# Performance work log

Hardware: AMD Instinct MI355X
Metric: run time of the kernel (lower is better)

Reference implementation:

```python
import jax, jax.numpy as jnp
import numpy as np
import math

B = 256          # batch size
D = 128          # input_size (embed dim)
N = 500000       # output_size == num_samples (memory bank rows)
K = 2048         # num_negative_samples
T = 0.07         # temperature
MOM = 0.5        # momentum
EPS = 1e-07


def _l2norm(x):
    return x / jnp.linalg.norm(x, axis=-1, keepdims=True)


def setup_inputs() -> dict:
    key = jax.random.key(0)
    k1, k2, k3, k4, k5, k6 = jax.random.split(key, 6)
    stdv = 1.0 / math.sqrt(D / 3.0)
    memory_v1 = jax.random.uniform(k1, (N, D), dtype=jnp.float32) * (2 * stdv) - stdv
    memory_v2 = jax.random.uniform(k2, (N, D), dtype=jnp.float32) * (2 * stdv) - stdv
    # embeds come out of an L2-normalization module in the original pipeline
    student_embed = _l2norm(jax.random.normal(k3, (B, D), dtype=jnp.float32))
    teacher_embed = _l2norm(jax.random.normal(k4, (B, D), dtype=jnp.float32))
    pos_idx = jax.random.randint(k5, (B,), 0, N, dtype=jnp.int64)
    contrast_idx = jax.random.randint(k6, (B, K + 1), 0, N, dtype=jnp.int64)
    contrast_idx = contrast_idx.at[:, 0].set(pos_idx)  # column 0 holds the positive
    return {
        'student_embed': student_embed,
        'teacher_embed': teacher_embed,
        'memory_v1': memory_v1,
        'memory_v2': memory_v2,
        'pos_idx': pos_idx,
        'contrast_idx': contrast_idx,
    }


def _contrast_loss(x):
    # x: [B, K+1] normalized exp-similarities; column 0 is the positive
    m = x.shape[1] - 1
    pn = 1.0 / float(N)  # num_samples
    noise = m * pn + EPS
    p_pos = x[:, 0]
    log_d1 = jnp.log(p_pos / (p_pos + noise))
    p_neg = x[:, 1:]
    log_d0 = jnp.log((m * pn) / (p_neg + noise))
    return -(log_d1.sum() + log_d0.sum()) / x.shape[0]


def reference(student_embed, teacher_embed, memory_v1, memory_v2, pos_idx, contrast_idx):
    output_size = memory_v1.shape[0]
    # gather [B, K+1, D] rows from each bank (detached in original)
    w1 = jax.lax.stop_gradient(memory_v1[contrast_idx])
    w2 = jax.lax.stop_gradient(memory_v2[contrast_idx])
    # per-sample bmm + exp/div  (teacher scored against v1 bank, student against v2)
    out_v2 = jnp.exp(jnp.einsum('bkd,bd->bk', w1, teacher_embed) / T)
    out_v1 = jnp.exp(jnp.einsum('bkd,bd->bk', w2, student_embed) / T)
    # first-call normalization constants (treated as constants thereafter)
    z_v1 = jax.lax.stop_gradient(out_v1.mean() * output_size)
    z_v2 = jax.lax.stop_gradient(out_v2.mean() * output_size)
    out_v1 = out_v1 / z_v1
    out_v2 = out_v2 / z_v2
    # momentum-weighted renormalize-and-scatter memory update (no_grad)
    s = jax.lax.stop_gradient(student_embed)
    t = jax.lax.stop_gradient(teacher_embed)
    l_pos = memory_v1[pos_idx] * MOM + s * (1.0 - MOM)
    updated_v1 = l_pos / jnp.sqrt((l_pos ** 2).sum(1, keepdims=True))
    new_memory_v1 = memory_v1.at[pos_idx].set(updated_v1)
    ab_pos = memory_v2[pos_idx] * MOM + t * (1.0 - MOM)
    updated_v2 = ab_pos / jnp.sqrt((ab_pos ** 2).sum(1, keepdims=True))
    new_memory_v2 = memory_v2.at[pos_idx].set(updated_v2)
    loss = _contrast_loss(out_v1) + _contrast_loss(out_v2)
    return loss, new_memory_v1, new_memory_v2
```

## Files before the change

### kernel.cpp

```cpp
#include <hip/hip_runtime.h>
#include <math.h>

namespace {
constexpr int kB = 256;
constexpr int kD = 128;
constexpr int kN = 500000;
constexpr int kKC = 2049;
constexpr int kNPair = kB * kKC;
constexpr float kTInv = 1.0f / 0.07f;
constexpr float kMom = 0.5f;
constexpr int kRB = 256;
constexpr long long kM = (long long)kN * kD;
constexpr long long kTot = 2 * kM;
constexpr int kChunk = 2048;
constexpr int kNB1 = (kN + kChunk - 1) / kChunk;
constexpr int kRows = 32;
constexpr int kTPB = kN / kRows;
constexpr int kTiles = 2 * kTPB;
constexpr int kLdsStride = 132;
constexpr int kTilesPerBlock = 16;
constexpr int kGrid8 = (kTiles + kTilesPerBlock - 1) / kTilesPerBlock;
}


__global__ __launch_bounds__(256) void hist_kernel(const int* __restrict__ cidx, int* __restrict__ A)
{
    int i = blockIdx.x * 256 + threadIdx.x;
    if (i < kNPair) atomicAdd(&A[cidx[i]], 1);
}

__global__ __launch_bounds__(256) void scan1_kernel(const int* __restrict__ A, int* __restrict__ bsum)
{
    long long base = (long long)blockIdx.x * kChunk;
    int t = threadIdx.x;
    int s = 0;
    #pragma unroll
    for (int j = 0; j < 8; ++j) {
        long long i = base + t * 8 + j;
        if (i < kN) s += A[i];
    }
    __shared__ int lds[256];
    lds[t] = s; __syncthreads();
    for (int st = 128; st > 0; st >>= 1) {
        if (t < st) lds[t] += lds[t + st];
        __syncthreads();
    }
    if (t == 0) bsum[blockIdx.x] = lds[0];
}

__global__ __launch_bounds__(256) void scan2_kernel(
    const int* __restrict__ bsum, int* __restrict__ bpre, int* __restrict__ offs)
{
    int t = threadIdx.x;
    int v = (t < kNB1) ? bsum[t] : 0;
    __shared__ int lds[256];
    lds[t] = v; __syncthreads();
    for (int st = 1; st < 256; st <<= 1) {
        int add = (t >= st) ? lds[t - st] : 0;
        __syncthreads();
        lds[t] += add;
        __syncthreads();
    }
    if (t < kNB1) bpre[t] = lds[t] - v;
    if (t == kNB1 - 1) offs[kN] = lds[t];
}

__global__ __launch_bounds__(256) void scan3_kernel(
    const int* __restrict__ A, const int* __restrict__ bpre, int* __restrict__ offs)
{
    int t = threadIdx.x;
    long long base = (long long)blockIdx.x * kChunk;
    int c[8]; int s = 0;
    #pragma unroll
    for (int j = 0; j < 8; ++j) {
        long long i = base + t * 8 + j;
        c[j] = (i < kN) ? A[i] : 0;
        s += c[j];
    }
    __shared__ int lds[256];
    lds[t] = s; __syncthreads();
    for (int st = 1; st < 256; st <<= 1) {
        int add = (t >= st) ? lds[t - st] : 0;
        __syncthreads();
        lds[t] += add;
        __syncthreads();
    }
    int excl = lds[t] - s + bpre[blockIdx.x];
    #pragma unroll
    for (int j = 0; j < 8; ++j) {
        long long i = base + t * 8 + j;
        if (i < kN) { offs[i] = excl; excl += c[j]; }
    }
}

__global__ __launch_bounds__(256) void scatter_kernel(
    const int* __restrict__ cidx, const int* __restrict__ offs,
    int* __restrict__ cur, long long* __restrict__ sorted64)
{
    int p = blockIdx.x * 256 + threadIdx.x;
    if (p < kNPair) {
        int r = cidx[p];
        int pos = offs[r] + atomicAdd(&cur[r], 1);
        sorted64[pos] = ((long long)r << 20) | (long long)p;
    }
}

__global__ __launch_bounds__(256) void fused8_kernel(
    const float* __restrict__ mem1, const float* __restrict__ mem2,
    const float* __restrict__ teacher, const float* __restrict__ student,
    const int* __restrict__ offs, const long long* __restrict__ sorted64,
    float* __restrict__ out, float* __restrict__ e2, float* __restrict__ e1)
{
    __shared__ float tile[kRows * kLdsStride];
    const int tid = threadIdx.x;
    const int lane = tid & 63;
    const int w = tid >> 6;
    float4* ov = reinterpret_cast<float4*>(out);

    if (blockIdx.x == 0 && tid == 0) out[kTot] = mem2[kM - 1];

    const int T0 = blockIdx.x * kTilesPerBlock;
    int T1 = T0 + kTilesPerBlock; if (T1 > kTiles) T1 = kTiles;

    for (int T = T0; T < T1; ++T) {
        const int bk = (T >= kTPB) ? 1 : 0;
        const int tt = T - bk * kTPB;
        const int r0 = tt * kRows;

        {
            const float4* bank4 = reinterpret_cast<const float4*>(bk ? mem2 : mem1);
            const long long lb4 = (long long)tt * (kRows * kD / 4) + w * 256;
            float4 v[4];
            #pragma unroll
            for (int i = 0; i < 4; ++i) v[i] = bank4[lb4 + i * 64 + lane];

            const long long gbase = (long long)bk * kM + (long long)r0 * kD
                                    + (long long)w * 1024;
            float carry = 0.f;
            if (gbase > 0) {
                long long g = gbase - 1;
                carry = (g < kM) ? mem1[g] : mem2[g - kM];
            }
            const long long g4 = gbase >> 2;
            #pragma unroll
            for (int i = 0; i < 4; ++i) {
                float4 c = v[i];
                int lr = w * 8 + i * 2 + (lane >> 5);
                *reinterpret_cast<float4*>(&tile[lr * kLdsStride + (lane & 31) * 4]) = c;
                float pw = __shfl_up(c.w, 1);
                if (lane == 0) pw = carry;
                carry = __shfl(c.w, 63);
                long long k4 = g4 + i * 64 + lane;
                if (k4 != 0) {
                    ov[k4] = make_float4(pw, c.x, c.y, c.z);
                } else {
                    out[1] = c.x; out[2] = c.y; out[3] = c.z;
                }
            }
        }
        __syncthreads();

        {
            const int o0  = offs[r0];
            const int cnt = offs[r0 + kRows] - o0;
            const float4* emb4 =
                reinterpret_cast<const float4*>(bk ? student : teacher);
            float* ep = bk ? e1 : e2;
            for (int t = tid; t < cnt; t += 256) {
                long long v = sorted64[o0 + t];
                int p  = (int)(v & 0xFFFFF);
                int lr = (int)(v >> 20) - r0;
                unsigned bb = (unsigned)p / (unsigned)kKC;
                const float4* er = emb4 + (long long)bb * 32;
                const float* row = &tile[lr * kLdsStride];
                float ax = 0.f, ay = 0.f, az = 0.f, aw = 0.f;
                #pragma unroll 8
                for (int kk = 0; kk < 32; ++kk) {
                    float4 rv = *reinterpret_cast<const float4*>(&row[kk * 4]);
                    float4 ev = er[kk];
                    ax += rv.x * ev.x; ay += rv.y * ev.y;
                    az += rv.z * ev.z; aw += rv.w * ev.w;
                }
                ep[p] = __expf((ax + ay + az + aw) * kTInv);
            }
        }
        __syncthreads();
    }
}


__global__ __launch_bounds__(256) void dots_kernel(
    const float* __restrict__ mem1, const float* __restrict__ mem2,
    const float* __restrict__ teacher, const float* __restrict__ student,
    const int* __restrict__ cidx,
    float* __restrict__ e2, float* __restrict__ e1)
{
    int gtid = blockIdx.x * 256 + threadIdx.x;
    int wave = gtid >> 6;
    int lane = threadIdx.x & 63;
    if (wave >= kNPair) return;
    int b = wave / kKC;
    long long row = (long long)cidx[wave] * kD;
    const float2 m1 = *reinterpret_cast<const float2*>(mem1 + row + lane * 2);
    const float2 m2 = *reinterpret_cast<const float2*>(mem2 + row + lane * 2);
    const float2 tv = *reinterpret_cast<const float2*>(teacher + b * kD + lane * 2);
    const float2 sv = *reinterpret_cast<const float2*>(student + b * kD + lane * 2);
    float d1 = m1.x * tv.x + m1.y * tv.y;
    float d2 = m2.x * sv.x + m2.y * sv.y;
    #pragma unroll
    for (int off = 32; off > 0; off >>= 1) {
        d1 += __shfl_xor(d1, off);
        d2 += __shfl_xor(d2, off);
    }
    if (lane == 0) {
        e2[wave] = __expf(d1 * kTInv);
        e1[wave] = __expf(d2 * kTInv);
    }
}

__global__ __launch_bounds__(256) void copy_kernel(
    const float* __restrict__ mem1, const float* __restrict__ mem2,
    float* __restrict__ out)
{
    const long long NV4 = (kTot + 1) / 4;
    const long long KS  = kM / 4;
    const float4* m1v = reinterpret_cast<const float4*>(mem1);
    const float4* m2v = reinterpret_cast<const float4*>(mem2);
    float4* ov = reinterpret_cast<float4*>(out);
    long long stride = (long long)gridDim.x * 256;
    for (long long k = (long long)blockIdx.x * 256 + threadIdx.x; k < NV4; k += stride) {
        if (k == 0) {
            out[1] = mem1[0]; out[2] = mem1[1]; out[3] = mem1[2];
            out[kTot] = mem2[kM - 1];
            continue;
        }
        float4 r;
        if (k < KS) {
            float4 a = m1v[k - 1];
            float4 b = m1v[k];
            r = make_float4(a.w, b.x, b.y, b.z);
        } else if (k == KS) {
            r = make_float4(mem1[kM - 1], mem2[0], mem2[1], mem2[2]);
        } else {
            float4 a = m2v[k - KS - 1];
            float4 b = m2v[k - KS];
            r = make_float4(a.w, b.x, b.y, b.z);
        }
        ov[k] = r;
    }
}


__global__ __launch_bounds__(256) void sums_kernel(
    const float* __restrict__ e2, const float* __restrict__ e1,
    float* __restrict__ p2, float* __restrict__ p1)
{
    __shared__ float s2[256], s1[256];
    float a2 = 0.f, a1 = 0.f;
    for (int i = blockIdx.x * 256 + threadIdx.x; i < kNPair; i += 256 * kRB) {
        a2 += e2[i];
        a1 += e1[i];
    }
    s2[threadIdx.x] = a2; s1[threadIdx.x] = a1;
    __syncthreads();
    for (int st = 128; st > 0; st >>= 1) {
        if ((int)threadIdx.x < st) {
            s2[threadIdx.x] += s2[threadIdx.x + st];
            s1[threadIdx.x] += s1[threadIdx.x + st];
        }
        __syncthreads();
    }
    if (threadIdx.x == 0) { p2[blockIdx.x] = s2[0]; p1[blockIdx.x] = s1[0]; }
}

__global__ __launch_bounds__(256) void z_kernel(
    const float* __restrict__ p2, const float* __restrict__ p1, float* __restrict__ z)
{
    __shared__ float s2[256], s1[256];
    s2[threadIdx.x] = p2[threadIdx.x];
    s1[threadIdx.x] = p1[threadIdx.x];
    __syncthreads();
    for (int st = 128; st > 0; st >>= 1) {
        if ((int)threadIdx.x < st) {
            s2[threadIdx.x] += s2[threadIdx.x + st];
            s1[threadIdx.x] += s1[threadIdx.x + st];
        }
        __syncthreads();
    }
    if (threadIdx.x == 0) {
        const float scale = (float)kN / (float)kNPair;
        z[0] = s2[0] * scale;
        z[1] = s1[0] * scale;
    }
}

__global__ __launch_bounds__(256) void lossp_kernel(
    const float* __restrict__ e2, const float* __restrict__ e1,
    const float* __restrict__ z, float* __restrict__ lp)
{
    const float mpn = 2048.0f / 500000.0f;
    const float noise = mpn + 1e-7f;
    const float iz2 = 1.0f / z[0];
    const float iz1 = 1.0f / z[1];
    float acc = 0.f;
    for (int i = blockIdx.x * 256 + threadIdx.x; i < kNPair; i += 256 * kRB) {
        int k = i % kKC;
        float x2 = e2[i] * iz2;
        float x1 = e1[i] * iz1;
        if (k == 0) {
            acc += __logf(x2 / (x2 + noise)) + __logf(x1 / (x1 + noise));
        } else {
            acc += __logf(mpn / (x2 + noise)) + __logf(mpn / (x1 + noise));
        }
    }
    __shared__ float s[256];
    s[threadIdx.x] = acc;
    __syncthreads();
    for (int st = 128; st > 0; st >>= 1) {
        if ((int)threadIdx.x < st) s[threadIdx.x] += s[threadIdx.x + st];
        __syncthreads();
    }
    if (threadIdx.x == 0) lp[blockIdx.x] = s[0];
}

__global__ __launch_bounds__(256) void final_kernel(
    const float* __restrict__ lp, float* __restrict__ out)
{
    __shared__ float s[256];
    s[threadIdx.x] = lp[threadIdx.x];
    __syncthreads();
    for (int st = 128; st > 0; st >>= 1) {
        if ((int)threadIdx.x < st) s[threadIdx.x] += s[threadIdx.x + st];
        __syncthreads();
    }
    if (threadIdx.x == 0) out[0] = -s[0] / (float)kB;
}


__global__ __launch_bounds__(64) void update_kernel(
    const float* __restrict__ mem1, const float* __restrict__ mem2,
    const float* __restrict__ student, const float* __restrict__ teacher,
    const int* __restrict__ pos_idx,
    float* __restrict__ out1, float* __restrict__ out2)
{
    int b = blockIdx.x;
    int lane = threadIdx.x;
    int p = pos_idx[b];
    for (int b2 = b + 1; b2 < kB; ++b2)
        if (pos_idx[b2] == p) return;
    long long row = (long long)p * kD;
    float2 m1 = *reinterpret_cast<const float2*>(mem1 + row + lane * 2);
    float2 m2 = *reinterpret_cast<const float2*>(mem2 + row + lane * 2);
    float2 sv = *reinterpret_cast<const float2*>(student + b * kD + lane * 2);
    float2 tv = *reinterpret_cast<const float2*>(teacher + b * kD + lane * 2);
    float2 l1 = make_float2(m1.x * kMom + sv.x * (1.f - kMom),
                            m1.y * kMom + sv.y * (1.f - kMom));
    float2 l2 = make_float2(m2.x * kMom + tv.x * (1.f - kMom),
                            m2.y * kMom + tv.y * (1.f - kMom));
    float n1 = l1.x * l1.x + l1.y * l1.y;
    float n2 = l2.x * l2.x + l2.y * l2.y;
    #pragma unroll
    for (int off = 32; off > 0; off >>= 1) {
        n1 += __shfl_xor(n1, off);
        n2 += __shfl_xor(n2, off);
    }
    float i1 = 1.0f / sqrtf(n1);
    float i2 = 1.0f / sqrtf(n2);
    out1[row + lane * 2]     = l1.x * i1;
    out1[row + lane * 2 + 1] = l1.y * i1;
    out2[row + lane * 2]     = l2.x * i2;
    out2[row + lane * 2 + 1] = l2.y * i2;
}

extern "C" void kernel_launch(void* const* d_in, const int* in_sizes, int n_in,
                              void* d_out, int out_size, void* d_ws, size_t ws_size,
                              hipStream_t stream) {
    const float* student = (const float*)d_in[0];
    const float* teacher = (const float*)d_in[1];
    const float* mem1    = (const float*)d_in[2];
    const float* mem2    = (const float*)d_in[3];
    const int*   pos_idx = (const int*)d_in[4];
    const int*   cidx    = (const int*)d_in[5];

    float* out  = (float*)d_out;
    float* out1 = out + 1;
    float* out2 = out + 1 + kM;

    float* ws = (float*)d_ws;
    float* e2 = ws;
    float* e1 = e2 + kNPair;
    long long* sorted64 = (long long*)(e1 + kNPair);
    float* p2 = (float*)(sorted64 + kNPair);
    float* p1 = p2 + kRB;
    float* zz = p1 + kRB;
    float* lp = zz + 2;
    int*   A    = (int*)(lp + kRB);
    int*   cur  = A + kN;
    int*   offs = cur + kN;
    int*   bsum = offs + kN + 1;
    int*   bpre = bsum + kNB1;
    size_t need = (size_t)((char*)(bpre + kNB1) - (char*)d_ws);

    if (ws_size >= need) {
        hipMemsetAsync(A, 0, 2 * (size_t)kN * sizeof(int), stream);
        hist_kernel<<<(kNPair + 255) / 256, 256, 0, stream>>>(cidx, A);
        scan1_kernel<<<kNB1, 256, 0, stream>>>(A, bsum);
        scan2_kernel<<<1, 256, 0, stream>>>(bsum, bpre, offs);
        scan3_kernel<<<kNB1, 256, 0, stream>>>(A, bpre, offs);
        scatter_kernel<<<(kNPair + 255) / 256, 256, 0, stream>>>(cidx, offs, cur, sorted64);
        fused8_kernel<<<kGrid8, 256, 0, stream>>>(mem1, mem2, teacher, student,
                                                  offs, sorted64, out, e2, e1);
    } else {
        int nblocks = (kNPair + 3) / 4;
        dots_kernel<<<nblocks, 256, 0, stream>>>(mem1, mem2, teacher, student, cidx, e2, e1);
        copy_kernel<<<2048, 256, 0, stream>>>(mem1, mem2, out);
    }

    sums_kernel<<<kRB, 256, 0, stream>>>(e2, e1, p2, p1);
    z_kernel<<<1, 256, 0, stream>>>(p2, p1, zz);
    lossp_kernel<<<kRB, 256, 0, stream>>>(e2, e1, zz, lp);
    final_kernel<<<1, 256, 0, stream>>>(lp, out);
    update_kernel<<<kB, 64, 0, stream>>>(mem1, mem2, student, teacher, pos_idx, out1, out2);
}
```

Baseline: 359.0 us.

## Software-pipeline tile loads and sorted-index prefetch in fused bank kernel

The fused copy-and-dot kernel now prefetches the next tile's bank rows, carry value and sorted index list into registers and a double-buffered LDS array while the current tile is processed, so global load latency overlaps with compute. The dot products are split across 4 lanes per pair with a rotated column order and shuffle reduction, instead of one thread per pair. Full syncthreads are replaced by explicit waitcnt plus s_barrier with sched_barrier fences. In exchange it raises register and LDS use and adds manual scheduling that relies on the chosen wait counts being correct.

```diff
diff --git a/kernel.cpp b/kernel.cpp
--- a/kernel.cpp
+++ b/kernel.cpp
@@ -19,7 +19,7 @@
 constexpr int kTiles = 2 * kTPB;
 constexpr int kLdsStride = 132;
 constexpr int kTilesPerBlock = 16;
-constexpr int kGrid8 = (kTiles + kTilesPerBlock - 1) / kTilesPerBlock;
+constexpr int kGrid9 = (kTiles + kTilesPerBlock - 1) / kTilesPerBlock;
 }
 
 
@@ -105,13 +105,14 @@
     }
 }
 
-__global__ __launch_bounds__(256) void fused8_kernel(
+__global__ __launch_bounds__(256) void fused9_kernel(
     const float* __restrict__ mem1, const float* __restrict__ mem2,
     const float* __restrict__ teacher, const float* __restrict__ student,
     const int* __restrict__ offs, const long long* __restrict__ sorted64,
     float* __restrict__ out, float* __restrict__ e2, float* __restrict__ e1)
 {
     __shared__ float tile[kRows * kLdsStride];
+    __shared__ long long s64lds[2][256];
     const int tid = threadIdx.x;
     const int lane = tid & 63;
     const int w = tid >> 6;
@@ -121,36 +122,85 @@
 
     const int T0 = blockIdx.x * kTilesPerBlock;
     int T1 = T0 + kTilesPerBlock; if (T1 > kTiles) T1 = kTiles;
-
-    for (int T = T0; T < T1; ++T) {
+    const int nT = T1 - T0;
+
+    auto r0of = [](int T) { return (T >= kTPB) ? (T - kTPB) * kRows : T * kRows; };
+
+    int rA = r0of(T0);
+    int oA = offs[rA];
+    int cA = offs[rA + kRows] - oA;
+    int TB = (1 < nT) ? T0 + 1 : T0;
+    int rB = r0of(TB);
+    int oB = offs[rB];
+    int cB = (1 < nT) ? (offs[rB + kRows] - oB) : 0;
+    {
+        long long v = 0;
+        if (tid < cA) v = sorted64[oA + tid];
+        s64lds[0][tid] = v;
+    }
+    float4 sl0, sl1, sl2, sl3;
+    float carry;
+    {
+        int bk = (T0 >= kTPB);
+        const float4* bank4 = reinterpret_cast<const float4*>(bk ? mem2 : mem1);
+        long long lb4 = (long long)(bk ? T0 - kTPB : T0) * (kRows * kD / 4) + w * 256;
+        sl0 = bank4[lb4 + 0 * 64 + lane];
+        sl1 = bank4[lb4 + 1 * 64 + lane];
+        sl2 = bank4[lb4 + 2 * 64 + lane];
+        sl3 = bank4[lb4 + 3 * 64 + lane];
+        long long gb = (long long)bk * kM + (long long)rA * kD + (long long)w * 1024;
+        carry = 0.f;
+        if (gb > 0) { long long g = gb - 1; carry = (g < kM) ? mem1[g] : mem2[g - kM]; }
+    }
+
+    for (int i = 0; i < nT; ++i) {
+        const int T = T0 + i;
+        const int cur = i & 1;
         const int bk = (T >= kTPB) ? 1 : 0;
-        const int tt = T - bk * kTPB;
-        const int r0 = tt * kRows;
-
+        const int r0 = r0of(T);
+        const int o0 = oA, cnt = cA;
+
+        float4 sn0, sn1, sn2, sn3;
+        float carryn;
         {
-            const float4* bank4 = reinterpret_cast<const float4*>(bk ? mem2 : mem1);
-            const long long lb4 = (long long)tt * (kRows * kD / 4) + w * 256;
-            float4 v[4];
-            #pragma unroll
-            for (int i = 0; i < 4; ++i) v[i] = bank4[lb4 + i * 64 + lane];
-
+            int Tn = (i + 1 < nT) ? T + 1 : T;
+            int bkn = (Tn >= kTPB);
+            const float4* bank4 = reinterpret_cast<const float4*>(bkn ? mem2 : mem1);
+            long long lb4 = (long long)(bkn ? Tn - kTPB : Tn) * (kRows * kD / 4) + w * 256;
+            sn0 = bank4[lb4 + 0 * 64 + lane];
+            sn1 = bank4[lb4 + 1 * 64 + lane];
+            sn2 = bank4[lb4 + 2 * 64 + lane];
+            sn3 = bank4[lb4 + 3 * 64 + lane];
+            long long gb = (long long)bkn * kM + (long long)r0of(Tn) * kD + (long long)w * 1024;
+            carryn = 0.f;
+            if (gb > 0) { long long g = gb - 1; carryn = (g < kM) ? mem1[g] : mem2[g - kM]; }
+        }
+        long long s64n = 0;
+        if (tid < cB) s64n = sorted64[oB + tid];
+        int oC, cC;
+        {
+            int Tn2 = (i + 2 < nT) ? T + 2 : T;
+            int rn2 = r0of(Tn2);
+            oC = offs[rn2];
+            cC = (i + 2 < nT) ? (offs[rn2 + kRows] - oC) : 0;
+        }
+        __builtin_amdgcn_sched_barrier(0);
+
+        {
             const long long gbase = (long long)bk * kM + (long long)r0 * kD
                                     + (long long)w * 1024;
-            float carry = 0.f;
-            if (gbase > 0) {
-                long long g = gbase - 1;
-                carry = (g < kM) ? mem1[g] : mem2[g - kM];
-            }
             const long long g4 = gbase >> 2;
+            float cr = carry;
+            float4 v[4] = {sl0, sl1, sl2, sl3};
             #pragma unroll
-            for (int i = 0; i < 4; ++i) {
-                float4 c = v[i];
-                int lr = w * 8 + i * 2 + (lane >> 5);
+            for (int i2 = 0; i2 < 4; ++i2) {
+                float4 c = v[i2];
+                int lr = w * 8 + i2 * 2 + (lane >> 5);
                 *reinterpret_cast<float4*>(&tile[lr * kLdsStride + (lane & 31) * 4]) = c;
                 float pw = __shfl_up(c.w, 1);
-                if (lane == 0) pw = carry;
-                carry = __shfl(c.w, 63);
-                long long k4 = g4 + i * 64 + lane;
+                if (lane == 0) pw = cr;
+                cr = __shfl(c.w, 63);
+                long long k4 = g4 + i2 * 64 + lane;
                 if (k4 != 0) {
                     ov[k4] = make_float4(pw, c.x, c.y, c.z);
                 } else {
@@ -158,33 +208,47 @@
                 }
             }
         }
-        __syncthreads();
+        asm volatile("s_waitcnt lgkmcnt(0)" ::: "memory");
+        __builtin_amdgcn_sched_barrier(0);
+        __builtin_amdgcn_s_barrier();
+        __builtin_amdgcn_sched_barrier(0);
 
         {
-            const int o0  = offs[r0];
-            const int cnt = offs[r0 + kRows] - o0;
-            const float4* emb4 =
-                reinterpret_cast<const float4*>(bk ? student : teacher);
+            s64lds[cur ^ 1][tid] = s64n;
+
+            const float4* emb4 = reinterpret_cast<const float4*>(bk ? student : teacher);
             float* ep = bk ? e1 : e2;
-            for (int t = tid; t < cnt; t += 256) {
-                long long v = sorted64[o0 + t];
+            const int sub = tid & 3;
+            for (int t = tid >> 2; t < cnt; t += 64) {
+                long long v = (t < 256) ? s64lds[cur][t] : sorted64[o0 + t];
                 int p  = (int)(v & 0xFFFFF);
                 int lr = (int)(v >> 20) - r0;
-                unsigned bb = (unsigned)p / (unsigned)kKC;
-                const float4* er = emb4 + (long long)bb * 32;
-                const float* row = &tile[lr * kLdsStride];
+                const float4* er = emb4
+                    + (long long)((unsigned)p / (unsigned)kKC) * 32 + sub * 8;
+                const float* row = &tile[lr * kLdsStride + sub * 32];
                 float ax = 0.f, ay = 0.f, az = 0.f, aw = 0.f;
-                #pragma unroll 8
-                for (int kk = 0; kk < 32; ++kk) {
-                    float4 rv = *reinterpret_cast<const float4*>(&row[kk * 4]);
-                    float4 ev = er[kk];
+                #pragma unroll
+                for (int kk = 0; kk < 8; ++kk) {
+                    int c4 = (kk + sub * 2) & 7;
+                    float4 ev = er[c4];
+                    float4 rv = *reinterpret_cast<const float4*>(&row[c4 * 4]);
                     ax += rv.x * ev.x; ay += rv.y * ev.y;
                     az += rv.z * ev.z; aw += rv.w * ev.w;
                 }
-                ep[p] = __expf((ax + ay + az + aw) * kTInv);
+                float d = (ax + ay) + (az + aw);
+                d += __shfl_xor(d, 1);
+                d += __shfl_xor(d, 2);
+                if (sub == 0) ep[p] = __expf(d * kTInv);
             }
         }
-        __syncthreads();
+        __builtin_amdgcn_sched_barrier(0);
+        asm volatile("s_waitcnt lgkmcnt(0)" ::: "memory");
+        __builtin_amdgcn_s_barrier();
+        __builtin_amdgcn_sched_barrier(0);
+
+        sl0 = sn0; sl1 = sn1; sl2 = sn2; sl3 = sn3;
+        carry = carryn;
+        oA = oB; cA = cB; oB = oC; cB = cC;
     }
 }
 
@@ -408,7 +472,7 @@
         scan2_kernel<<<1, 256, 0, stream>>>(bsum, bpre, offs);
         scan3_kernel<<<kNB1, 256, 0, stream>>>(A, bpre, offs);
         scatter_kernel<<<(kNPair + 255) / 256, 256, 0, stream>>>(cidx, offs, cur, sorted64);
-        fused8_kernel<<<kGrid8, 256, 0, stream>>>(mem1, mem2, teacher, student,
+        fused9_kernel<<<kGrid9, 256, 0, stream>>>(mem1, mem2, teacher, student,
                                                   offs, sorted64, out, e2, e1);
     } else {
         int nblocks = (kNPair + 3) / 4;
```

Result: faster. 323.2 us (-10.0%).
